# Performance work log

Hardware: AMD Instinct MI355X
Metric: run time of the kernel (lower is better)

Reference implementation:

```python
import jax, jax.numpy as jnp
import numpy as np

NHEAD = 16  # n_head; head_size N = C // NHEAD = 64


def _forward(x, time_maa_x, time_maa, time_maa_w1, time_maa_w2,
             time_decay, time_decay_w1, time_decay_w2,
             time_aaaaa, time_aaa_w1, time_aaa_w2,
             time_kkk_w1, time_kkk_w2,
             gate_w1, gate_w2,
             time_misc_a, ma_w1, ma_w2,
             time_misc_k, mk_w1, mk_w2,
             receptance, key_w, value, output,
             ln_w, ln_b, time_faaaa):
    B, T, C = x.shape
    H, N = NHEAD, C // NHEAD
    # --- fused_time_shift: token shift + 4-way LoRA mixing (rg, wa, k, v) ---
    xprev = jnp.pad(x, ((0, 0), (1, 0), (0, 0)))[:, :T]   # shift right by one token
    xx = xprev - x
    xxx = x + xx * time_maa_x
    mix = jnp.tanh(xxx @ time_maa_w1.T).reshape(B, T, 4, -1)        # (B,T,4,32)
    deltas = jnp.einsum('btfd,fcd->fbtc', mix, time_maa_w2)         # (4,B,T,C)
    xrg, xwa, xk, xv = x[None] + xx[None] * (time_maa + deltas)
    # --- projections + small LoRAs ---
    r = xrg @ receptance.T
    g = jnp.tanh(xrg @ gate_w1.T) @ gate_w2.T                       # gate
    k = xk @ key_w.T
    kk1 = jnp.tanh(xk @ time_kkk_w1.T)
    mk1 = xk @ mk_w1.T
    v = xv @ value.T
    w1 = jnp.tanh(xwa @ time_decay_w1.T)
    a1 = xwa @ time_aaa_w1.T
    ma1 = xwa @ ma_w1.T
    # data-dependent log-decay, clamped <= -0.5 via softplus
    w = -jax.nn.softplus(-(time_decay + w1 @ time_decay_w2.T)) - 0.5
    # removal key kk: per-head L2-normalized
    kk = k + kk1 @ time_kkk_w2.T
    kk = kk.reshape(B, T, H, N)
    kk = kk / jnp.maximum(jnp.linalg.norm(kk, axis=-1, keepdims=True), 1e-12)
    kk = kk.reshape(B, T, C)
    a = jax.nn.sigmoid(time_aaaaa + a1 @ time_aaa_w2.T)
    ma = jax.nn.sigmoid(time_misc_a + ma1 @ ma_w2.T)
    k = k * ma + k * a * (1 - ma)
    mk = jax.nn.sigmoid(time_misc_k + mk1 @ mk_w2.T)
    k = k * jnp.exp(w * mk)
    b = -kk * a
    # --- RWKV-7 linear-attention scan; state S: (B,H,N_value,N_key) ---
    def heads(z):
        return z.reshape(B, T, H, N).transpose(1, 0, 2, 3)          # (T,B,H,N)
    rh, wh, kh, vh, kkh, bh = map(heads, (r, w, k, v, kk, b))

    def step(S, inp):
        r_, w_, k_, v_, kk_, b_ = inp
        sab = jnp.einsum('bhvk,bhk->bhv', S, kk_)                   # S @ kk
        S = (S * jnp.exp(w_)[:, :, None, :]                         # diag decay on key dim
             + sab[..., None] * b_[:, :, None, :]                   # (S kk) b^T  (delta-rule removal)
             + v_[..., None] * k_[:, :, None, :])                   # v k^T
        y = jnp.einsum('bhvk,bhk->bhv', S, r_)
        return S, y

    S0 = jnp.zeros((B, H, N, N), x.dtype)
    _, y = jax.lax.scan(step, S0, (rh, wh, kh, vh, kkh, bh))
    y = y.transpose(1, 0, 2, 3)                                     # (B,T,H,N)
    # --- GroupNorm (H groups, eps=64e-5) + r.k bonus + gate (fused_attn_ln tail) ---
    mu = y.mean(-1, keepdims=True)
    var = ((y - mu) ** 2).mean(-1, keepdims=True)
    yn = (y - mu) / jnp.sqrt(var + 0.00064) * ln_w.reshape(H, N) + ln_b.reshape(H, N)
    r4 = r.reshape(B, T, H, N)
    k4 = k.reshape(B, T, H, N)
    v4 = v.reshape(B, T, H, N)
    bonus = (r4 * k4 * time_faaaa.reshape(H, N)).sum(-1, keepdims=True) * v4
    out = (yn + bonus).reshape(B, T, C) * g
    return out @ output.T


def setup_inputs() -> dict:
    key = jax.random.key(0)
    ks = iter(jax.random.split(key, 40))
    B, T, C = 2, 1024, 1024
    def n(shape, s=1.0):
        return jax.random.normal(next(ks), shape, jnp.float32) * s
    def u(shape, lo, hi):
        return jax.random.uniform(next(ks), shape, jnp.float32, lo, hi)
    d = {}
    d['x'] = n((B, T, C))
    d['time_maa_x'] = u((1, 1, C), 0.0, 1.0)
    d['time_maa'] = u((4, 1, 1, C), 0.0, 1.0)
    d['time_maa_w1'] = n((128, C), 0.02)
    d['time_maa_w2'] = n((4, C, 32), 0.05)
    d['time_decay'] = u((1, 1, C), -6.5, -1.5)
    d['time_decay_w1'] = n((64, C), 0.02)
    d['time_decay_w2'] = n((C, 64), 0.05)
    d['time_aaaaa'] = n((1, 1, C), 0.1)
    d['time_aaa_w1'] = n((16, C), 0.02)
    d['time_aaa_w2'] = n((C, 16), 0.05)
    d['time_kkk_w1'] = n((16, C), 0.02)
    d['time_kkk_w2'] = n((C, 16), 0.05)
    d['gate_w1'] = n((128, C), 0.05)
    d['gate_w2'] = n((C, 128), 0.05)
    d['time_misc_a'] = n((1, 1, C), 0.1)
    d['ma_w1'] = n((16, C), 0.02)
    d['ma_w2'] = n((C, 16), 0.05)
    d['time_misc_k'] = n((1, 1, C), 0.1)
    d['mk_w1'] = n((16, C), 0.02)
    d['mk_w2'] = n((C, 16), 0.05)
    s = 0.5 / C ** 0.5
    d['receptance'] = u((C, C), -s, s)
    d['key_w'] = u((C, C), -0.1 * s, 0.1 * s)
    d['value'] = u((C, C), -s, s)
    d['output'] = n((C, C), 0.02)
    d['ln_w'] = jnp.ones((C,), jnp.float32)
    d['ln_b'] = jnp.zeros((C,), jnp.float32)
    d['time_faaaa'] = n((C,), 0.1)
    return d


def reference(x, time_maa_x, time_maa, time_maa_w1, time_maa_w2,
              time_decay, time_decay_w1, time_decay_w2,
              time_aaaaa, time_aaa_w1, time_aaa_w2,
              time_kkk_w1, time_kkk_w2,
              gate_w1, gate_w2,
              time_misc_a, ma_w1, ma_w2,
              time_misc_k, mk_w1, mk_w2,
              receptance, key_w, value, output,
              ln_w, ln_b, time_faaaa):
    return _forward(x, time_maa_x, time_maa, time_maa_w1, time_maa_w2,
                    time_decay, time_decay_w1, time_decay_w2,
                    time_aaaaa, time_aaa_w1, time_aaa_w2,
                    time_kkk_w1, time_kkk_w2,
                    gate_w1, gate_w2,
                    time_misc_a, ma_w1, ma_w2,
                    time_misc_k, mk_w1, mk_w2,
                    receptance, key_w, value, output,
                    ln_w, ln_b, time_faaaa)
```

## Files before the change

kernel.cpp:

```cpp
#include <hip/hip_runtime.h>
#include <hip/hip_bf16.h>

typedef __hip_bfloat16 bf16;

#define B_ 2
#define T_ 1024
#define C_ 1024
#define H_ 16
#define N_ 64

using short4v = __attribute__((ext_vector_type(4))) short;
using short8 = __attribute__((ext_vector_type(8))) short;
using f32x4 = __attribute__((ext_vector_type(4))) float;

__device__ __forceinline__ float us2f(unsigned short u) {
  return __uint_as_float(((unsigned int)u) << 16);
}
__device__ __forceinline__ float bs2f(short s) {
  return __uint_as_float(((unsigned int)(unsigned short)s) << 16);
}
__device__ __forceinline__ bf16 f2bf(float f) { return __float2bfloat16(f); }
__device__ __forceinline__ short bfbits(float f) {
  bf16 h = __float2bfloat16(f);
  return *reinterpret_cast<short*>(&h);
}
__device__ __forceinline__ float sigmoidf_(float x) { return 1.0f / (1.0f + expf(-x)); }
__device__ __forceinline__ float softplusf_(float x) {
  return fmaxf(x, 0.0f) + log1pf(expf(-fabsf(x)));
}
__device__ __forceinline__ float qsum16(float x) {
  int a = __builtin_amdgcn_update_dpp(0, __float_as_int(x), 0xB1, 0xF, 0xF, true);
  x += __int_as_float(a);
  int b = __builtin_amdgcn_update_dpp(0, __float_as_int(x), 0x4E, 0xF, 0xF, true);
  x += __int_as_float(b);
  int c = __builtin_amdgcn_update_dpp(0, __float_as_int(x), 0x124, 0xF, 0xF, true);
  x += __int_as_float(c);
  int d = __builtin_amdgcn_update_dpp(0, __float_as_int(x), 0x128, 0xF, 0xF, true);
  x += __int_as_float(d);
  return x;
}
__device__ __forceinline__ void qsum16x2(float& x, float& y) {
  int a0 = __builtin_amdgcn_update_dpp(0, __float_as_int(x), 0xB1, 0xF, 0xF, true);
  int b0 = __builtin_amdgcn_update_dpp(0, __float_as_int(y), 0xB1, 0xF, 0xF, true);
  x += __int_as_float(a0); y += __int_as_float(b0);
  int a1 = __builtin_amdgcn_update_dpp(0, __float_as_int(x), 0x4E, 0xF, 0xF, true);
  int b1 = __builtin_amdgcn_update_dpp(0, __float_as_int(y), 0x4E, 0xF, 0xF, true);
  x += __int_as_float(a1); y += __int_as_float(b1);
  int a2 = __builtin_amdgcn_update_dpp(0, __float_as_int(x), 0x124, 0xF, 0xF, true);
  int b2 = __builtin_amdgcn_update_dpp(0, __float_as_int(y), 0x124, 0xF, 0xF, true);
  x += __int_as_float(a2); y += __int_as_float(b2);
  int a3 = __builtin_amdgcn_update_dpp(0, __float_as_int(x), 0x128, 0xF, 0xF, true);
  int b3 = __builtin_amdgcn_update_dpp(0, __float_as_int(y), 0x128, 0xF, 0xF, true);
  x += __int_as_float(a3); y += __int_as_float(b3);
}

__global__ __launch_bounds__(256) void cvt_all_kernel(
    const float* __restrict__ s0, const float* __restrict__ s1,
    const float* __restrict__ s2, const float* __restrict__ s3,
    const float* __restrict__ s4, const float* __restrict__ s5,
    const float* __restrict__ s6,
    bf16* __restrict__ d0, bf16* __restrict__ d1, bf16* __restrict__ d2,
    bf16* __restrict__ d3, bf16* __restrict__ d4, bf16* __restrict__ d5,
    bf16* __restrict__ d6,
    const float* __restrict__ tkw1, const float* __restrict__ mkw1,
    const float* __restrict__ tdw1, const float* __restrict__ taw1,
    const float* __restrict__ maw1,
    bf16* __restrict__ wsk, bf16* __restrict__ wswa,
    const float* __restrict__ tmw2, const float* __restrict__ tdw2,
    const float* __restrict__ tkw2, const float* __restrict__ taw2,
    const float* __restrict__ maw2, const float* __restrict__ mkw2,
    bf16* __restrict__ tmw2e, bf16* __restrict__ tdw2b,
    bf16* __restrict__ tkw2b, bf16* __restrict__ taw2b,
    bf16* __restrict__ maw2b, bf16* __restrict__ mkw2b) {
  long bidx = blockIdx.x;
  const float* s; bf16* d; long off;
  if (bidx < 4480) {
    long i4 = bidx * 256 + threadIdx.x;
    if (i4 < 32768) { s = s0; d = d0; off = i4; }
    else if (i4 < 294912) { s = s1; d = d1; off = i4 - 32768; }
    else if (i4 < 327680) { s = s2; d = d2; off = i4 - 294912; }
    else if (i4 < 360448) { s = s3; d = d3; off = i4 - 327680; }
    else if (i4 < 622592) { s = s4; d = d4; off = i4 - 360448; }
    else if (i4 < 884736) { s = s5; d = d5; off = i4 - 622592; }
    else { s = s6; d = d6; off = i4 - 884736; }
  } else if (bidx < 4608) {
    long i4 = (bidx - 4480) * 256 + threadIdx.x;
    long so, dof;
    if (i4 < 4096) { s = tkw1; so = i4; d = wsk; dof = i4; }
    else if (i4 < 8192) { s = mkw1; so = i4 - 4096; d = wsk; dof = i4; }
    else if (i4 < 24576) { s = tdw1; so = i4 - 8192; d = wswa; dof = i4 - 8192; }
    else if (i4 < 28672) { s = taw1; so = i4 - 24576; d = wswa; dof = i4 - 8192; }
    else { s = maw1; so = i4 - 28672; d = wswa; dof = i4 - 8192; }
    float4 v = *(const float4*)(s + so * 4);
    d[dof * 4 + 0] = f2bf(v.x); d[dof * 4 + 1] = f2bf(v.y);
    d[dof * 4 + 2] = f2bf(v.z); d[dof * 4 + 3] = f2bf(v.w);
    return;
  } else if (bidx < 4736) {
    long i4 = (bidx - 4608) * 256 + threadIdx.x;
    if (i4 < 16384) { s = tdw2; d = tdw2b; off = i4; }
    else if (i4 < 20480) { s = tkw2; d = tkw2b; off = i4 - 16384; }
    else if (i4 < 24576) { s = taw2; d = taw2b; off = i4 - 20480; }
    else if (i4 < 28672) { s = maw2; d = maw2b; off = i4 - 24576; }
    else { s = mkw2; d = mkw2b; off = i4 - 28672; }
  } else {
    long i4 = (bidx - 4736) * 256 + threadIdx.x;
    long n = i4 >> 5;
    int k0 = (int)(i4 & 31) << 2;
    int f = (int)(n >> 10);
    float4 v = {0.f, 0.f, 0.f, 0.f};
    if ((k0 >> 5) == f) v = *(const float4*)(tmw2 + n * 32 + (k0 & 31));
    tmw2e[i4 * 4 + 0] = f2bf(v.x);
    tmw2e[i4 * 4 + 1] = f2bf(v.y);
    tmw2e[i4 * 4 + 2] = f2bf(v.z);
    tmw2e[i4 * 4 + 3] = f2bf(v.w);
    return;
  }
  float4 v = *(const float4*)(s + off * 4);
  d[off * 4 + 0] = f2bf(v.x);
  d[off * 4 + 1] = f2bf(v.y);
  d[off * 4 + 2] = f2bf(v.z);
  d[off * 4 + 3] = f2bf(v.w);
}

struct GemmBatch {
  const bf16* A[6]; const bf16* W[6];
  float* Cf[6]; bf16* Cb[6];
  int N[6]; int actN[6];
};

__global__ __launch_bounds__(256) void gemm_batch_kernel(GemmBatch gb, int K) {
  __shared__ __align__(16) bf16 As[128][72];
  __shared__ __align__(16) bf16 Ws[64][72];
  int z = blockIdx.z;
  int Nz = gb.N[z];
  int n0 = blockIdx.x << 6;
  if (n0 >= Nz) return;
  int m0 = blockIdx.y << 7;
  int actN = gb.actN[z];
  const bf16* A = gb.A[z];
  const bf16* W = gb.W[z];
  float* Cf = gb.Cf[z];
  bf16* Cb = gb.Cb[z];
  int tid = threadIdx.x;
  int arow = tid >> 1, acol = (tid & 1) << 5;
  int wrow = tid >> 2, wcol = (tid & 3) << 4;
  int wv = tid >> 6, lane = tid & 63;
  int fr = lane & 15, fq = lane >> 4;
  bool wok = (n0 + wrow) < Nz;
  const bf16* Ap = A + (long)(m0 + arow) * K + acol;
  const bf16* Wp = W + (long)(n0 + wrow) * K + wcol;
  short8 zz = {0, 0, 0, 0, 0, 0, 0, 0};
  f32x4 a00 = {0.f, 0.f, 0.f, 0.f};
  f32x4 a01 = a00, a02 = a00, a03 = a00, a10 = a00, a11 = a00, a12 = a00, a13 = a00;
  for (int k0 = 0; k0 < K; k0 += 64) {
    *(short8*)&As[arow][acol] = *(const short8*)(Ap + k0);
    *(short8*)&As[arow][acol + 8] = *(const short8*)(Ap + k0 + 8);
    *(short8*)&As[arow][acol + 16] = *(const short8*)(Ap + k0 + 16);
    *(short8*)&As[arow][acol + 24] = *(const short8*)(Ap + k0 + 24);
    *(short8*)&Ws[wrow][wcol] = wok ? *(const short8*)(Wp + k0) : zz;
    *(short8*)&Ws[wrow][wcol + 8] = wok ? *(const short8*)(Wp + k0 + 8) : zz;
    __syncthreads();
#pragma unroll
    for (int kk = 0; kk < 2; kk++) {
      int ko = (fq << 3) + (kk << 5);
      short8 af0 = *(const short8*)&As[(wv << 5) + fr][ko];
      short8 af1 = *(const short8*)&As[(wv << 5) + 16 + fr][ko];
      short8 b0 = *(const short8*)&Ws[fr][ko];
      short8 b1 = *(const short8*)&Ws[16 + fr][ko];
      short8 b2 = *(const short8*)&Ws[32 + fr][ko];
      short8 b3 = *(const short8*)&Ws[48 + fr][ko];
      a00 = __builtin_amdgcn_mfma_f32_16x16x32_bf16(af0, b0, a00, 0, 0, 0);
      a01 = __builtin_amdgcn_mfma_f32_16x16x32_bf16(af0, b1, a01, 0, 0, 0);
      a02 = __builtin_amdgcn_mfma_f32_16x16x32_bf16(af0, b2, a02, 0, 0, 0);
      a03 = __builtin_amdgcn_mfma_f32_16x16x32_bf16(af0, b3, a03, 0, 0, 0);
      a10 = __builtin_amdgcn_mfma_f32_16x16x32_bf16(af1, b0, a10, 0, 0, 0);
      a11 = __builtin_amdgcn_mfma_f32_16x16x32_bf16(af1, b1, a11, 0, 0, 0);
      a12 = __builtin_amdgcn_mfma_f32_16x16x32_bf16(af1, b2, a12, 0, 0, 0);
      a13 = __builtin_amdgcn_mfma_f32_16x16x32_bf16(af1, b3, a13, 0, 0, 0);
    }
    __syncthreads();
  }
  int ocol = n0 + fr;
  int orow0 = m0 + (wv << 5) + (fq << 2);
#define WRB(accv, mf, nt) { int col = ocol + ((nt) << 4); if (col < Nz) { \
    _Pragma("unroll") for (int r = 0; r < 4; r++) { \
      float vvv = accv[r]; if (col < actN) vvv = tanhf(vvv); \
      long oi = (long)(orow0 + ((mf) << 4) + r) * Nz + col; \
      if (Cb) Cb[oi] = f2bf(vvv); else Cf[oi] = vvv; } } }
  WRB(a00, 0, 0) WRB(a01, 0, 1) WRB(a02, 0, 2) WRB(a03, 0, 3)
  WRB(a10, 1, 0) WRB(a11, 1, 1) WRB(a12, 1, 2) WRB(a13, 1, 3)
#undef WRB
}

__global__ __launch_bounds__(256) void gemm_mix_kernel(
    const float* __restrict__ x, const float* __restrict__ tmx,
    const bf16* __restrict__ W, bf16* __restrict__ Cb) {
  __shared__ __align__(16) bf16 As[128][72];
  __shared__ __align__(16) bf16 Ws[64][72];
  const int K = 1024;
  int n0 = blockIdx.x << 6;
  int m0 = blockIdx.y << 7;
  int tid = threadIdx.x;
  int arow = tid >> 1, acol = (tid & 1) << 5;
  int wrow = tid >> 2, wcol = (tid & 3) << 4;
  int wv = tid >> 6, lane = tid & 63;
  int fr = lane & 15, fq = lane >> 4;
  int grow = m0 + arow;
  int t = grow & (T_ - 1);
  const float* xp = x + (long)grow * C_ + acol;
  const bf16* Wp = W + (long)(n0 + wrow) * K + wcol;
  f32x4 a00 = {0.f, 0.f, 0.f, 0.f};
  f32x4 a01 = a00, a02 = a00, a03 = a00, a10 = a00, a11 = a00, a12 = a00, a13 = a00;
  for (int k0 = 0; k0 < K; k0 += 64) {
#pragma unroll
    for (int jj = 0; jj < 4; jj++) {
      int co = k0 + (jj << 3);
      float4 c0 = *(const float4*)(xp + co);
      float4 c1 = *(const float4*)(xp + co + 4);
      float4 q0 = {0.f, 0.f, 0.f, 0.f}, q1 = q0;
      if (t > 0) {
        q0 = *(const float4*)(xp + co - C_);
        q1 = *(const float4*)(xp + co + 4 - C_);
      }
      float4 m0v = *(const float4*)(tmx + co + acol);
      float4 m1v = *(const float4*)(tmx + co + acol + 4);
      short8 sv;
      sv[0] = bfbits(fmaf(q0.x - c0.x, m0v.x, c0.x));
      sv[1] = bfbits(fmaf(q0.y - c0.y, m0v.y, c0.y));
      sv[2] = bfbits(fmaf(q0.z - c0.z, m0v.z, c0.z));
      sv[3] = bfbits(fmaf(q0.w - c0.w, m0v.w, c0.w));
      sv[4] = bfbits(fmaf(q1.x - c1.x, m1v.x, c1.x));
      sv[5] = bfbits(fmaf(q1.y - c1.y, m1v.y, c1.y));
      sv[6] = bfbits(fmaf(q1.z - c1.z, m1v.z, c1.z));
      sv[7] = bfbits(fmaf(q1.w - c1.w, m1v.w, c1.w));
      *(short8*)&As[arow][acol + (jj << 3)] = sv;
    }
    *(short8*)&Ws[wrow][wcol] = *(const short8*)(Wp + k0);
    *(short8*)&Ws[wrow][wcol + 8] = *(const short8*)(Wp + k0 + 8);
    __syncthreads();
#pragma unroll
    for (int kk = 0; kk < 2; kk++) {
      int ko = (fq << 3) + (kk << 5);
      short8 af0 = *(const short8*)&As[(wv << 5) + fr][ko];
      short8 af1 = *(const short8*)&As[(wv << 5) + 16 + fr][ko];
      short8 b0 = *(const short8*)&Ws[fr][ko];
      short8 b1 = *(const short8*)&Ws[16 + fr][ko];
      short8 b2 = *(const short8*)&Ws[32 + fr][ko];
      short8 b3 = *(const short8*)&Ws[48 + fr][ko];
      a00 = __builtin_amdgcn_mfma_f32_16x16x32_bf16(af0, b0, a00, 0, 0, 0);
      a01 = __builtin_amdgcn_mfma_f32_16x16x32_bf16(af0, b1, a01, 0, 0, 0);
      a02 = __builtin_amdgcn_mfma_f32_16x16x32_bf16(af0, b2, a02, 0, 0, 0);
      a03 = __builtin_amdgcn_mfma_f32_16x16x32_bf16(af0, b3, a03, 0, 0, 0);
      a10 = __builtin_amdgcn_mfma_f32_16x16x32_bf16(af1, b0, a10, 0, 0, 0);
      a11 = __builtin_amdgcn_mfma_f32_16x16x32_bf16(af1, b1, a11, 0, 0, 0);
      a12 = __builtin_amdgcn_mfma_f32_16x16x32_bf16(af1, b2, a12, 0, 0, 0);
      a13 = __builtin_amdgcn_mfma_f32_16x16x32_bf16(af1, b3, a13, 0, 0, 0);
    }
    __syncthreads();
  }
  const int Nz = 128;
  int ocol = n0 + fr;
  int orow0 = m0 + (wv << 5) + (fq << 2);
#define WRM(accv, mf, nt) { int col = ocol + ((nt) << 4); \
    _Pragma("unroll") for (int r = 0; r < 4; r++) { \
      long oi = (long)(orow0 + ((mf) << 4) + r) * Nz + col; \
      Cb[oi] = f2bf(tanhf(accv[r])); } }
  WRM(a00, 0, 0) WRM(a01, 0, 1) WRM(a02, 0, 2) WRM(a03, 0, 3)
  WRM(a10, 1, 0) WRM(a11, 1, 1) WRM(a12, 1, 2) WRM(a13, 1, 3)
#undef WRM
}

__global__ __launch_bounds__(256) void apply_mix_kernel(
    const float* __restrict__ x, const bf16* __restrict__ deltas,
    const float* __restrict__ tmaa,
    bf16* __restrict__ xrg, bf16* __restrict__ xwa,
    bf16* __restrict__ xk, bf16* __restrict__ xv) {
  long i4 = (long)blockIdx.x * 256 + threadIdx.x;
  int m = (int)(i4 >> 8);
  int cq = (int)(i4 & 255) << 2;
  int t = m & (T_ - 1);
  long xo = (long)m * C_ + cq;
  float4 xb = *(const float4*)(x + xo);
  float4 xp = {0.f, 0.f, 0.f, 0.f};
  if (t > 0) xp = *(const float4*)(x + xo - C_);
  float4 xxv = {xp.x - xb.x, xp.y - xb.y, xp.z - xb.z, xp.w - xb.w};
  bf16* outs[4] = {xrg, xwa, xk, xv};
#pragma unroll
  for (int f = 0; f < 4; f++) {
    short4v dl = *(const short4v*)(deltas + (long)m * 4096 + (f << 10) + cq);
    float4 ta = *(const float4*)(tmaa + f * C_ + cq);
    short4v sv;
    sv[0] = bfbits(fmaf(xxv.x, ta.x + bs2f(dl[0]), xb.x));
    sv[1] = bfbits(fmaf(xxv.y, ta.y + bs2f(dl[1]), xb.y));
    sv[2] = bfbits(fmaf(xxv.z, ta.z + bs2f(dl[2]), xb.z));
    sv[3] = bfbits(fmaf(xxv.w, ta.w + bs2f(dl[3]), xb.w));
    *(short4v*)(outs[f] + xo) = sv;
  }
}

__global__ __launch_bounds__(256) void fuse2_kernel(
    const float* __restrict__ kraw, const float* __restrict__ out1,
    const float* __restrict__ out2,
    const bf16* __restrict__ dw2, const bf16* __restrict__ kkw2,
    const bf16* __restrict__ aw2, const bf16* __restrict__ maw2,
    const bf16* __restrict__ mkw2,
    const float* __restrict__ tdec, const float* __restrict__ taa,
    const float* __restrict__ tma, const float* __restrict__ tmk,
    float* __restrict__ ew, float* __restrict__ kfin,
    float* __restrict__ kkn, float* __restrict__ bbo) {
  int m = blockIdx.x, tid = threadIdx.x;
  __shared__ float w1r[64], kk1r[16], a1r[16], ma1r[16], mk1r[16];
  if (tid < 64) w1r[tid] = out2[(long)m * 96 + tid];
  else if (tid < 80) kk1r[tid - 64] = out1[(long)m * 32 + (tid - 64)];
  else if (tid < 96) a1r[tid - 80] = out2[(long)m * 96 + 64 + (tid - 80)];
  else if (tid < 112) ma1r[tid - 96] = out2[(long)m * 96 + 80 + (tid - 96)];
  else if (tid < 128) mk1r[tid - 112] = out1[(long)m * 32 + 16 + (tid - 112)];
  __syncthreads();
  float kkp[4], av[4], wv[4], kr[4], mkv[4];
  float sumsq = 0.f;
#pragma unroll
  for (int j = 0; j < 4; j++) {
    int c = (tid << 2) + j;
    long off = (long)m * C_ + c;
    float wd = 0.f;
    const short8* dp = (const short8*)(dw2 + ((long)c << 6));
#pragma unroll
    for (int d8 = 0; d8 < 8; d8++) {
      short8 u = dp[d8];
      int db = d8 << 3;
#pragma unroll
      for (int e = 0; e < 8; e++) wd += w1r[db + e] * bs2f(u[e]);
    }
    float w = -softplusf_(-(tdec[c] + wd)) - 0.5f;
    wv[j] = w;
    float kd = 0.f, ad = 0.f, mad = 0.f, mkd = 0.f;
    const short8* kp = (const short8*)(kkw2 + ((long)c << 4));
    const short8* ap = (const short8*)(aw2 + ((long)c << 4));
    const short8* mp = (const short8*)(maw2 + ((long)c << 4));
    const short8* qp = (const short8*)(mkw2 + ((long)c << 4));
#pragma unroll
    for (int d8 = 0; d8 < 2; d8++) {
      short8 u1 = kp[d8], u2 = ap[d8], u3 = mp[d8], u4 = qp[d8];
      int db = d8 << 3;
#pragma unroll
      for (int e = 0; e < 8; e++) {
        kd += kk1r[db + e] * bs2f(u1[e]);
        ad += a1r[db + e] * bs2f(u2[e]);
        mad += ma1r[db + e] * bs2f(u3[e]);
        mkd += mk1r[db + e] * bs2f(u4[e]);
      }
    }
    float krw = kraw[off];
    float kkpre = krw + kd;
    kkp[j] = kkpre;
    sumsq += kkpre * kkpre;
    float a = sigmoidf_(taa[c] + ad);
    av[j] = a;
    float ma = sigmoidf_(tma[c] + mad);
    float mk = sigmoidf_(tmk[c] + mkd);
    mkv[j] = mk;
    kr[j] = krw * (ma + a * (1.f - ma));
  }
  sumsq += __shfl_xor(sumsq, 1);
  sumsq += __shfl_xor(sumsq, 2);
  sumsq += __shfl_xor(sumsq, 4);
  sumsq += __shfl_xor(sumsq, 8);
  float rn = 1.0f / fmaxf(sqrtf(sumsq), 1e-12f);
#pragma unroll
  for (int j = 0; j < 4; j++) {
    int c = (tid << 2) + j;
    long off = (long)m * C_ + c;
    float kknv = kkp[j] * rn;
    kkn[off] = kknv;
    bbo[off] = -kknv * av[j];
    ew[off] = expf(wv[j]);
    kfin[off] = kr[j] * expf(wv[j] * mkv[j]);
  }
}

#define SCHUNK 16
#define NCHUNK (T_ / SCHUNK)
__global__ __launch_bounds__(256, 1) void scan_kernel(
    const float* __restrict__ rB, const float* __restrict__ ewB,
    const float* __restrict__ kB, const float* __restrict__ vB,
    const float* __restrict__ kkB, const float* __restrict__ bbB,
    float* __restrict__ yB) {
  __shared__ __align__(16) float lds[2][6][SCHUNK * 64];
  int bid = blockIdx.x;
  int bh = bid >> 2, rg = bid & 3;
  int b = bh >> 4, h = bh & 15;
  int tid = threadIdx.x;
  int wave = tid >> 6, lane = tid & 63;
  int g = lane >> 4, q = lane & 15;
  int row = (rg << 4) + (wave << 2) + g;
  int kq = q << 2;
  const long base = ((long)b * T_) * C_ + (h << 6);
  const float* s0 = kkB + base;
  const float* s1 = ewB + base;
  const float* s2 = kB + base;
  const float* s3 = bbB + base;
  const float* s4 = rB + base;
  const float* s5 = vB + base;
  int stok = tid >> 4;
  int spc = (tid & 15) << 2;
  int lo = (stok << 6) + spc;
  float4 rb0, rb1, rb2, rb3, rb4, rb5;
  auto loadc = [&](int c) {
    long go = (long)((c << 4) + stok) * C_ + spc;
    rb0 = *(const float4*)(s0 + go);
    rb1 = *(const float4*)(s1 + go);
    rb2 = *(const float4*)(s2 + go);
    rb3 = *(const float4*)(s3 + go);
    rb4 = *(const float4*)(s4 + go);
    rb5 = *(const float4*)(s5 + go);
  };
  auto stage = [&](int buf) {
    *(float4*)&lds[buf][0][lo] = rb0;
    *(float4*)&lds[buf][1][lo] = rb1;
    *(float4*)&lds[buf][2][lo] = rb2;
    *(float4*)&lds[buf][3][lo] = rb3;
    *(float4*)&lds[buf][4][lo] = rb4;
    *(float4*)&lds[buf][5][lo] = rb5;
  };
  float S0 = 0.f, S1 = 0.f, S2 = 0.f, S3 = 0.f;
  float ypv = 0.f;
  float4 Q0kk, Q0ew, Q0k, Q0bb, Q0r; float Q0v;
  float4 Q1kk, Q1ew, Q1k, Q1bb, Q1r; float Q1v;
  float4 Q2kk, Q2ew, Q2k, Q2bb, Q2r; float Q2v;

#define PF(i, tt) { int tb_ = ((tt) << 6); \
    Q##i##kk = *(const float4*)&lds[cur][0][tb_ + kq]; \
    Q##i##ew = *(const float4*)&lds[cur][1][tb_ + kq]; \
    Q##i##k  = *(const float4*)&lds[cur][2][tb_ + kq]; \
    Q##i##bb = *(const float4*)&lds[cur][3][tb_ + kq]; \
    Q##i##r  = *(const float4*)&lds[cur][4][tb_ + kq]; \
    Q##i##v  = lds[cur][5][tb_ + row]; }
#define SBAR __builtin_amdgcn_sched_barrier(0x7)
#define ST(i, gtok, FIRSTT) { \
    float p_ = fmaf(S1, Q##i##kk.y, S0 * Q##i##kk.x) + \
               fmaf(S3, Q##i##kk.w, S2 * Q##i##kk.z); \
    float yo_ = ypv; \
    qsum16x2(p_, yo_); \
    if (q == 0 && !((FIRSTT) && c == 0)) \
      yB[base + (long)((gtok) - 1) * C_ + row] = yo_; \
    float n0 = fmaf(S0, Q##i##ew.x, Q##i##v * Q##i##k.x); \
    float n1 = fmaf(S1, Q##i##ew.y, Q##i##v * Q##i##k.y); \
    float n2 = fmaf(S2, Q##i##ew.z, Q##i##v * Q##i##k.z); \
    float n3 = fmaf(S3, Q##i##ew.w, Q##i##v * Q##i##k.w); \
    S0 = fmaf(p_, Q##i##bb.x, n0); \
    S1 = fmaf(p_, Q##i##bb.y, n1); \
    S2 = fmaf(p_, Q##i##bb.z, n2); \
    S3 = fmaf(p_, Q##i##bb.w, n3); \
    ypv = fmaf(S1, Q##i##r.y, S0 * Q##i##r.x) + \
          fmaf(S3, Q##i##r.w, S2 * Q##i##r.z); }

  loadc(0);
  stage(0);
  loadc(1);
  __syncthreads();
  int cur = 0;
// ... 14 lines not shown
    PF(1, 10); SBAR; ST(2, t0 + 8, false);
    PF(2, 11); SBAR; ST(0, t0 + 9, false);
    PF(0, 12); SBAR; ST(1, t0 + 10, false);
    PF(1, 13); SBAR; ST(2, t0 + 11, false);
    PF(2, 14); SBAR; ST(0, t0 + 12, false);
    PF(0, 15); SBAR; ST(1, t0 + 13, false);
    ST(2, t0 + 14, false);
    ST(0, t0 + 15, false);
    __syncthreads();
    cur ^= 1;
  }
  {
    float yo = qsum16(ypv);
    if (q == 0) yB[base + (long)(T_ - 1) * C_ + row] = yo;
  }
#undef PF
#undef SBAR
#undef ST
}

__global__ __launch_bounds__(256) void gnout_kernel(
    const float* __restrict__ y, const float* __restrict__ r,
    const float* __restrict__ kf, const float* __restrict__ v,
    const float* __restrict__ g,
    const float* __restrict__ lnw, const float* __restrict__ lnb,
    const float* __restrict__ fa, bf16* __restrict__ z) {
  int tid = threadIdx.x;
  int w = tid >> 6, lane = tid & 63;
  int gi = (blockIdx.x << 2) + w;
  int h = gi & 15, mt = gi >> 4;
  long off = (long)mt * C_ + (h << 6) + lane;
  float yv = y[off];
  float s = yv;
  s += __shfl_xor(s, 1); s += __shfl_xor(s, 2); s += __shfl_xor(s, 4);
  s += __shfl_xor(s, 8); s += __shfl_xor(s, 16); s += __shfl_xor(s, 32);
  float mu = s * (1.0f / 64.0f);
  float d = yv - mu;
  float s2 = d * d;
  s2 += __shfl_xor(s2, 1); s2 += __shfl_xor(s2, 2); s2 += __shfl_xor(s2, 4);
  s2 += __shfl_xor(s2, 8); s2 += __shfl_xor(s2, 16); s2 += __shfl_xor(s2, 32);
  float var = s2 * (1.0f / 64.0f);
  int hc = (h << 6) + lane;
  float dot = r[off] * kf[off] * fa[hc];
  dot += __shfl_xor(dot, 1); dot += __shfl_xor(dot, 2); dot += __shfl_xor(dot, 4);
  dot += __shfl_xor(dot, 8); dot += __shfl_xor(dot, 16); dot += __shfl_xor(dot, 32);
  float yn = d * rsqrtf(var + 0.00064f) * lnw[hc] + lnb[hc];
  z[off] = f2bf((yn + dot * v[off]) * g[off]);
}

extern "C" void kernel_launch(void* const* d_in, const int* in_sizes, int n_in,
                              void* d_out, int out_size, void* d_ws, size_t ws_size,
                              hipStream_t stream) {
  const float* x = (const float*)d_in[0];
  const float* tmx = (const float*)d_in[1];
  const float* tmaa = (const float*)d_in[2];
  const float* tmw1 = (const float*)d_in[3];
  const float* tmw2 = (const float*)d_in[4];
  const float* tdec = (const float*)d_in[5];
  const float* tdw1 = (const float*)d_in[6];
  const float* tdw2 = (const float*)d_in[7];
  const float* taa5 = (const float*)d_in[8];
  const float* taw1 = (const float*)d_in[9];
  const float* taw2 = (const float*)d_in[10];
  const float* tkw1 = (const float*)d_in[11];
  const float* tkw2 = (const float*)d_in[12];
  const float* gw1 = (const float*)d_in[13];
  const float* gw2 = (const float*)d_in[14];
  const float* tmia = (const float*)d_in[15];
  const float* maw1 = (const float*)d_in[16];
  const float* maw2 = (const float*)d_in[17];
  const float* tmik = (const float*)d_in[18];
  const float* mkw1 = (const float*)d_in[19];
  const float* mkw2 = (const float*)d_in[20];
  const float* wrec = (const float*)d_in[21];
  const float* wkey = (const float*)d_in[22];
  const float* wval = (const float*)d_in[23];
  const float* wout = (const float*)d_in[24];
  const float* lnw = (const float*)d_in[25];
  const float* lnb = (const float*)d_in[26];
  const float* faaa = (const float*)d_in[27];

  const long MT = 2048, CC = 1024;
  char* base = (char*)d_ws;
  float* xx = (float*)base;    base += MT * CC * 4;
  bf16* xxxb = (bf16*)base;    base += MT * CC * 2;
  bf16* xrgb = (bf16*)base;    base += MT * CC * 2;
  bf16* xwab = (bf16*)base;    base += MT * CC * 2;
  bf16* xkb = (bf16*)base;     base += MT * CC * 2;
  bf16* xvb = (bf16*)base;     base += MT * CC * 2;
  float* rr = (float*)base;    base += MT * CC * 4;
  float* kraw = (float*)base;  base += MT * CC * 4;
  float* vv = (float*)base;    base += MT * CC * 4;
  float* gg = (float*)base;    base += MT * CC * 4;
  float* bbo = (float*)base;   base += MT * CC * 4;
  float* mix = (float*)base;   base += MT * 128 * 4;
  bf16* g1b = (bf16*)base;     base += MT * 128 * 2;
  float* out1 = (float*)base;  base += MT * 32 * 4;
  float* out2 = (float*)base;  base += MT * 96 * 4;
  bf16* zb = (bf16*)base;      base += MT * CC * 2;
  bf16* tmw1b = (bf16*)base;   base += 128 * CC * 2;
  bf16* wrecb = (bf16*)base;   base += CC * CC * 2;
  bf16* gw1b = (bf16*)base;    base += 128 * CC * 2;
  bf16* gw2b = (bf16*)base;    base += CC * 128 * 2;
  bf16* wkeyb = (bf16*)base;   base += CC * CC * 2;
  bf16* wvalb = (bf16*)base;   base += CC * CC * 2;
  bf16* woutb = (bf16*)base;   base += CC * CC * 2;
  bf16* wskb = (bf16*)base;    base += 32 * CC * 2;
  bf16* wswab = (bf16*)base;   base += 96 * CC * 2;
  bf16* tmw2b = (bf16*)base;   base += 4 * CC * 32 * 2;
  bf16* tdw2b = (bf16*)base;   base += CC * 64 * 2;
  bf16* tkw2b = (bf16*)base;   base += CC * 16 * 2;
  bf16* taw2b = (bf16*)base;   base += CC * 16 * 2;
  bf16* maw2b = (bf16*)base;   base += CC * 16 * 2;
  bf16* mkw2b = (bf16*)base;   base += CC * 16 * 2;
  bf16* mixb = (bf16*)base;    base += MT * 128 * 2;
  bf16* tmw2e = (bf16*)base;   base += 4096L * 128 * 2;
  bf16* deltasb = (bf16*)base; base += MT * 4096L * 2;
  float* ew = kraw;
  float* kfin = (float*)xrgb;
  float* kkn = (float*)xkb;
  float* y = xx;
  (void)xxxb; (void)mix; (void)tmw2b;

  cvt_all_kernel<<<5248, 256, 0, stream>>>(
      tmw1, wrec, gw1, gw2, wkey, wval, wout,
      tmw1b, wrecb, gw1b, gw2b, wkeyb, wvalb, woutb,
      tkw1, mkw1, tdw1, taw1, maw1, wskb, wswab,
      tmw2, tdw2, tkw2, taw2, maw2, mkw2,
      tmw2e, tdw2b, tkw2b, taw2b, maw2b, mkw2b);

  gemm_mix_kernel<<<dim3(2, 16), 256, 0, stream>>>(x, tmx, tmw1b, mixb);
  {
    GemmBatch gb = {};
    gb.A[0] = mixb; gb.W[0] = tmw2e; gb.Cf[0] = nullptr; gb.Cb[0] = deltasb;
    gb.N[0] = 4096; gb.actN[0] = 0;
    gemm_batch_kernel<<<dim3(64, 16, 1), 256, 0, stream>>>(gb, 128);
  }
  apply_mix_kernel<<<2048, 256, 0, stream>>>(x, deltasb, tmaa,
                                             xrgb, xwab, xkb, xvb);
  {
    GemmBatch gb = {};
    gb.A[0] = xrgb; gb.W[0] = wrecb; gb.Cf[0] = rr;   gb.Cb[0] = nullptr; gb.N[0] = 1024; gb.actN[0] = 0;
    gb.A[1] = xrgb; gb.W[1] = gw1b;  gb.Cf[1] = nullptr; gb.Cb[1] = g1b;  gb.N[1] = 128;  gb.actN[1] = 128;
    gb.A[2] = xkb;  gb.W[2] = wkeyb; gb.Cf[2] = kraw; gb.Cb[2] = nullptr; gb.N[2] = 1024; gb.actN[2] = 0;
    gb.A[3] = xkb;  gb.W[3] = wskb;  gb.Cf[3] = out1; gb.Cb[3] = nullptr; gb.N[3] = 32;   gb.actN[3] = 16;
    gb.A[4] = xvb;  gb.W[4] = wvalb; gb.Cf[4] = vv;   gb.Cb[4] = nullptr; gb.N[4] = 1024; gb.actN[4] = 0;
    gb.A[5] = xwab; gb.W[5] = wswab; gb.Cf[5] = out2; gb.Cb[5] = nullptr; gb.N[5] = 96;   gb.actN[5] = 64;
    gemm_batch_kernel<<<dim3(16, 16, 6), 256, 0, stream>>>(gb, 1024);
  }
  {
    GemmBatch gb = {};
    gb.A[0] = g1b; gb.W[0] = gw2b; gb.Cf[0] = gg; gb.Cb[0] = nullptr;
    gb.N[0] = 1024; gb.actN[0] = 0;
    gemm_batch_kernel<<<dim3(16, 16, 1), 256, 0, stream>>>(gb, 128);
  }
  fuse2_kernel<<<2048, 256, 0, stream>>>(kraw, out1, out2,
                                         tdw2b, tkw2b, taw2b, maw2b, mkw2b,
                                         tdec, taa5, tmia, tmik,
                                         ew, kfin, kkn, bbo);
  scan_kernel<<<128, 256, 0, stream>>>(rr, ew, kfin, vv, kkn, bbo, y);
  gnout_kernel<<<8192, 256, 0, stream>>>(y, rr, kfin, vv, gg, lnw, lnb, faaa, zb);
  {
    GemmBatch gb = {};
    gb.A[0] = zb; gb.W[0] = woutb; gb.Cf[0] = (float*)d_out; gb.Cb[0] = nullptr;
    gb.N[0] = 1024; gb.actN[0] = 0;
    gemm_batch_kernel<<<dim3(16, 16, 1), 256, 0, stream>>>(gb, 1024);
  }
}
```

Measured before the change: 522.7 us.

## Fuse mix-delta GEMM with apply step and move small LoRA up-projections to MFMA GEMM

The deltas GEMM epilogue now applies the token-shift mixing directly, so the bf16 deltas buffer no longer goes through global memory and the separate apply kernel is gone. The five small second-stage LoRA projections (decay, a, ma, kkk, mk) are packed into a block-structured 5120x128 weight and computed by the batched MFMA GEMM, replacing scalar dot products inside fuse2. fuse2 then becomes a vectorised elementwise kernel that reads a large fp32 d2 buffer. The trade-off is extra zero-padded MFMA work and the traffic to write and read d2, plus an epilogue in the fused kernel that does scattered scalar x loads.

Result: faster. 429.5 us (-17.8%).

```diff
diff --git a/kernel.cpp b/kernel.cpp
--- a/kernel.cpp
+++ b/kernel.cpp
@@ -13,9 +13,6 @@
 using short8 = __attribute__((ext_vector_type(8))) short;
 using f32x4 = __attribute__((ext_vector_type(4))) float;
 
-__device__ __forceinline__ float us2f(unsigned short u) {
-  return __uint_as_float(((unsigned int)u) << 16);
-}
 __device__ __forceinline__ float bs2f(short s) {
   return __uint_as_float(((unsigned int)(unsigned short)s) << 16);
 }
@@ -59,7 +56,7 @@
     const float* __restrict__ s2, const float* __restrict__ s3,
     const float* __restrict__ s4, const float* __restrict__ s5,
     const float* __restrict__ s6,
-    bf16* __restrict__ d0, bf16* __restrict__ d1, bf16* __restrict__ d2,
+    bf16* __restrict__ d0, bf16* __restrict__ d1, bf16* __restrict__ d2w,
     bf16* __restrict__ d3, bf16* __restrict__ d4, bf16* __restrict__ d5,
     bf16* __restrict__ d6,
     const float* __restrict__ tkw1, const float* __restrict__ mkw1,
@@ -69,16 +66,14 @@
     const float* __restrict__ tmw2, const float* __restrict__ tdw2,
     const float* __restrict__ tkw2, const float* __restrict__ taw2,
     const float* __restrict__ maw2, const float* __restrict__ mkw2,
-    bf16* __restrict__ tmw2e, bf16* __restrict__ tdw2b,
-    bf16* __restrict__ tkw2b, bf16* __restrict__ taw2b,
-    bf16* __restrict__ maw2b, bf16* __restrict__ mkw2b) {
+    bf16* __restrict__ tmw2e, bf16* __restrict__ w2e5) {
   long bidx = blockIdx.x;
   const float* s; bf16* d; long off;
   if (bidx < 4480) {
     long i4 = bidx * 256 + threadIdx.x;
     if (i4 < 32768) { s = s0; d = d0; off = i4; }
     else if (i4 < 294912) { s = s1; d = d1; off = i4 - 32768; }
-    else if (i4 < 327680) { s = s2; d = d2; off = i4 - 294912; }
+    else if (i4 < 327680) { s = s2; d = d2w; off = i4 - 294912; }
     else if (i4 < 360448) { s = s3; d = d3; off = i4 - 327680; }
     else if (i4 < 622592) { s = s4; d = d4; off = i4 - 360448; }
     else if (i4 < 884736) { s = s5; d = d5; off = i4 - 622592; }
@@ -95,15 +90,8 @@
     d[dof * 4 + 0] = f2bf(v.x); d[dof * 4 + 1] = f2bf(v.y);
     d[dof * 4 + 2] = f2bf(v.z); d[dof * 4 + 3] = f2bf(v.w);
     return;
-  } else if (bidx < 4736) {
+  } else if (bidx < 5120) {
     long i4 = (bidx - 4608) * 256 + threadIdx.x;
-    if (i4 < 16384) { s = tdw2; d = tdw2b; off = i4; }
-    else if (i4 < 20480) { s = tkw2; d = tkw2b; off = i4 - 16384; }
-    else if (i4 < 24576) { s = taw2; d = taw2b; off = i4 - 20480; }
-    else if (i4 < 28672) { s = maw2; d = maw2b; off = i4 - 24576; }
-    else { s = mkw2; d = mkw2b; off = i4 - 28672; }
-  } else {
-    long i4 = (bidx - 4736) * 256 + threadIdx.x;
     long n = i4 >> 5;
     int k0 = (int)(i4 & 31) << 2;
     int f = (int)(n >> 10);
@@ -114,6 +102,23 @@
     tmw2e[i4 * 4 + 2] = f2bf(v.z);
     tmw2e[i4 * 4 + 3] = f2bf(v.w);
     return;
+  } else {
+    long i4 = (bidx - 5120) * 256 + threadIdx.x;
+    long rowi = i4 >> 5;
+    int k0 = (int)(i4 & 31) << 2;
+    int j = (int)(rowi >> 10);
+    int c = (int)(rowi & 1023);
+    float4 v = {0.f, 0.f, 0.f, 0.f};
+    if (j == 0) { if (k0 < 64) v = *(const float4*)(tdw2 + c * 64 + k0); }
+    else if (j == 1) { if (k0 >= 64 && k0 < 80) v = *(const float4*)(taw2 + c * 16 + (k0 - 64)); }
+    else if (j == 2) { if (k0 >= 80 && k0 < 96) v = *(const float4*)(maw2 + c * 16 + (k0 - 80)); }
+    else if (j == 3) { if (k0 >= 96 && k0 < 112) v = *(const float4*)(tkw2 + c * 16 + (k0 - 96)); }
+    else { if (k0 >= 112) v = *(const float4*)(mkw2 + c * 16 + (k0 - 112)); }
+    w2e5[i4 * 4 + 0] = f2bf(v.x);
+    w2e5[i4 * 4 + 1] = f2bf(v.y);
+    w2e5[i4 * 4 + 2] = f2bf(v.z);
+    w2e5[i4 * 4 + 3] = f2bf(v.w);
+    return;
   }
   float4 v = *(const float4*)(s + off * 4);
   d[off * 4 + 0] = f2bf(v.x);
@@ -125,7 +130,7 @@
 struct GemmBatch {
   const bf16* A[6]; const bf16* W[6];
   float* Cf[6]; bf16* Cb[6];
-  int N[6]; int actN[6];
+  int N[6]; int actN[6]; int ldc[6]; int coff[6];
 };
 
 __global__ __launch_bounds__(256) void gemm_batch_kernel(GemmBatch gb, int K) {
@@ -137,6 +142,7 @@
   if (n0 >= Nz) return;
   int m0 = blockIdx.y << 7;
   int actN = gb.actN[z];
+  int ldc = gb.ldc[z], coff = gb.coff[z];
   const bf16* A = gb.A[z];
   const bf16* W = gb.W[z];
   float* Cf = gb.Cf[z];
@@ -185,7 +191,7 @@
 #define WRB(accv, mf, nt) { int col = ocol + ((nt) << 4); if (col < Nz) { \
     _Pragma("unroll") for (int r = 0; r < 4; r++) { \
       float vvv = accv[r]; if (col < actN) vvv = tanhf(vvv); \
-      long oi = (long)(orow0 + ((mf) << 4) + r) * Nz + col; \
+      long oi = (long)(orow0 + ((mf) << 4) + r) * ldc + coff + col; \
       if (Cb) Cb[oi] = f2bf(vvv); else Cf[oi] = vvv; } } }
   WRB(a00, 0, 0) WRB(a01, 0, 1) WRB(a02, 0, 2) WRB(a03, 0, 3)
   WRB(a10, 1, 0) WRB(a11, 1, 1) WRB(a12, 1, 2) WRB(a13, 1, 3)
@@ -270,112 +276,140 @@
 #undef WRM
 }
 
-__global__ __launch_bounds__(256) void apply_mix_kernel(
-    const float* __restrict__ x, const bf16* __restrict__ deltas,
-    const float* __restrict__ tmaa,
+__global__ __launch_bounds__(256) void gemm_mixapply_kernel(
+    const bf16* __restrict__ A, const bf16* __restrict__ W,
+    const float* __restrict__ x, const float* __restrict__ tmaa,
     bf16* __restrict__ xrg, bf16* __restrict__ xwa,
     bf16* __restrict__ xk, bf16* __restrict__ xv) {
-  long i4 = (long)blockIdx.x * 256 + threadIdx.x;
-  int m = (int)(i4 >> 8);
-  int cq = (int)(i4 & 255) << 2;
-  int t = m & (T_ - 1);
-  long xo = (long)m * C_ + cq;
-  float4 xb = *(const float4*)(x + xo);
-  float4 xp = {0.f, 0.f, 0.f, 0.f};
-  if (t > 0) xp = *(const float4*)(x + xo - C_);
-  float4 xxv = {xp.x - xb.x, xp.y - xb.y, xp.z - xb.z, xp.w - xb.w};
-  bf16* outs[4] = {xrg, xwa, xk, xv};
+  __shared__ __align__(16) bf16 As[128][72];
+  __shared__ __align__(16) bf16 Ws[64][72];
+  const int K = 128;
+  int n0 = blockIdx.x << 6;
+  int m0 = blockIdx.y << 7;
+  int tid = threadIdx.x;
+  int arow = tid >> 1, acol = (tid & 1) << 5;
+  int wrow = tid >> 2, wcol = (tid & 3) << 4;
+  int wv = tid >> 6, lane = tid & 63;
+  int fr = lane & 15, fq = lane >> 4;
+  const bf16* Ap = A + (long)(m0 + arow) * K + acol;
+  const bf16* Wp = W + (long)(n0 + wrow) * K + wcol;
+  f32x4 a00 = {0.f, 0.f, 0.f, 0.f};
+  f32x4 a01 = a00, a02 = a00, a03 = a00, a10 = a00, a11 = a00, a12 = a00, a13 = a00;
+  for (int k0 = 0; k0 < K; k0 += 64) {
+    *(short8*)&As[arow][acol] = *(const short8*)(Ap + k0);
+    *(short8*)&As[arow][acol + 8] = *(const short8*)(Ap + k0 + 8);
+    *(short8*)&As[arow][acol + 16] = *(const short8*)(Ap + k0 + 16);
+    *(short8*)&As[arow][acol + 24] = *(const short8*)(Ap + k0 + 24);
+    *(short8*)&Ws[wrow][wcol] = *(const short8*)(Wp + k0);
+    *(short8*)&Ws[wrow][wcol + 8] = *(const short8*)(Wp + k0 + 8);
+    __syncthreads();
 #pragma unroll
-  for (int f = 0; f < 4; f++) {
-    short4v dl = *(const short4v*)(deltas + (long)m * 4096 + (f << 10) + cq);
-    float4 ta = *(const float4*)(tmaa + f * C_ + cq);
-    short4v sv;
-    sv[0] = bfbits(fmaf(xxv.x, ta.x + bs2f(dl[0]), xb.x));
-    sv[1] = bfbits(fmaf(xxv.y, ta.y + bs2f(dl[1]), xb.y));
-    sv[2] = bfbits(fmaf(xxv.z, ta.z + bs2f(dl[2]), xb.z));
-    sv[3] = bfbits(fmaf(xxv.w, ta.w + bs2f(dl[3]), xb.w));
-    *(short4v*)(outs[f] + xo) = sv;
-  }
+    for (int kk = 0; kk < 2; kk++) {
+      int ko = (fq << 3) + (kk << 5);
+      short8 af0 = *(const short8*)&As[(wv << 5) + fr][ko];
+      short8 af1 = *(const short8*)&As[(wv << 5) + 16 + fr][ko];
+      short8 b0 = *(const short8*)&Ws[fr][ko];
+      short8 b1 = *(const short8*)&Ws[16 + fr][ko];
+      short8 b2 = *(const short8*)&Ws[32 + fr][ko];
+      short8 b3 = *(const short8*)&Ws[48 + fr][ko];
+      a00 = __builtin_amdgcn_mfma_f32_16x16x32_bf16(af0, b0, a00, 0, 0, 0);
+      a01 = __builtin_amdgcn_mfma_f32_16x16x32_bf16(af0, b1, a01, 0, 0, 0);
+      a02 = __builtin_amdgcn_mfma_f32_16x16x32_bf16(af0, b2, a02, 0, 0, 0);
+      a03 = __builtin_amdgcn_mfma_f32_16x16x32_bf16(af0, b3, a03, 0, 0, 0);
+      a10 = __builtin_amdgcn_mfma_f32_16x16x32_bf16(af1, b0, a10, 0, 0, 0);
+      a11 = __builtin_amdgcn_mfma_f32_16x16x32_bf16(af1, b1, a11, 0, 0, 0);
+      a12 = __builtin_amdgcn_mfma_f32_16x16x32_bf16(af1, b2, a12, 0, 0, 0);
+      a13 = __builtin_amdgcn_mfma_f32_16x16x32_bf16(af1, b3, a13, 0, 0, 0);
+    }
+    __syncthreads();
+  }
+  int f = n0 >> 10;
+  int c0 = n0 & 1023;
+  bf16* outp = (f == 0) ? xrg : (f == 1) ? xwa : (f == 2) ? xk : xv;
+  int ocol = c0 + fr;
+  int orow0 = m0 + (wv << 5) + (fq << 2);
+#define WRA(accv, mf, nt) { int cc = ocol + ((nt) << 4); \
+    float ta = tmaa[(f << 10) + cc]; \
+    _Pragma("unroll") for (int r = 0; r < 4; r++) { \
+      int row = orow0 + ((mf) << 4) + r; \
+      int t = row & (T_ - 1); \
+      long xo = (long)row * C_ + cc; \
+      float xb = x[xo]; \
+      float xq = (t > 0) ? x[xo - C_] : 0.0f; \
+      outp[xo] = f2bf(fmaf(xq - xb, ta + accv[r], xb)); } }
+  WRA(a00, 0, 0) WRA(a01, 0, 1) WRA(a02, 0, 2) WRA(a03, 0, 3)
+  WRA(a10, 1, 0) WRA(a11, 1, 1) WRA(a12, 1, 2) WRA(a13, 1, 3)
+#undef WRA
 }
 
 __global__ __launch_bounds__(256) void fuse2_kernel(
-    const float* __restrict__ kraw, const float* __restrict__ out1,
-    const float* __restrict__ out2,
-    const bf16* __restrict__ dw2, const bf16* __restrict__ kkw2,
-    const bf16* __restrict__ aw2, const bf16* __restrict__ maw2,
-    const bf16* __restrict__ mkw2,
+    const float* __restrict__ kraw, const float* __restrict__ d2,
     const float* __restrict__ tdec, const float* __restrict__ taa,
     const float* __restrict__ tma, const float* __restrict__ tmk,
     float* __restrict__ ew, float* __restrict__ kfin,
     float* __restrict__ kkn, float* __restrict__ bbo) {
   int m = blockIdx.x, tid = threadIdx.x;
-  __shared__ float w1r[64], kk1r[16], a1r[16], ma1r[16], mk1r[16];
-  if (tid < 64) w1r[tid] = out2[(long)m * 96 + tid];
-  else if (tid < 80) kk1r[tid - 64] = out1[(long)m * 32 + (tid - 64)];
-  else if (tid < 96) a1r[tid - 80] = out2[(long)m * 96 + 64 + (tid - 80)];
-  else if (tid < 112) ma1r[tid - 96] = out2[(long)m * 96 + 80 + (tid - 96)];
-  else if (tid < 128) mk1r[tid - 112] = out1[(long)m * 32 + 16 + (tid - 112)];
-  __syncthreads();
-  float kkp[4], av[4], wv[4], kr[4], mkv[4];
+  int c4 = tid << 2;
+  const float* dp = d2 + (long)m * 5120;
+  float4 wd4 = *(const float4*)(dp + c4);
+  float4 ad4 = *(const float4*)(dp + 1024 + c4);
+  float4 mad4 = *(const float4*)(dp + 2048 + c4);
+  float4 kd4 = *(const float4*)(dp + 3072 + c4);
+  float4 mkd4 = *(const float4*)(dp + 4096 + c4);
+  float4 kraw4 = *(const float4*)(kraw + (long)m * C_ + c4);
+  float4 tdec4 = *(const float4*)(tdec + c4);
+  float4 taa4 = *(const float4*)(taa + c4);
+  float4 tma4 = *(const float4*)(tma + c4);
+  float4 tmk4 = *(const float4*)(tmk + c4);
+  float wd[4] = {wd4.x, wd4.y, wd4.z, wd4.w};
+  float ad[4] = {ad4.x, ad4.y, ad4.z, ad4.w};
+  float mad[4] = {mad4.x, mad4.y, mad4.z, mad4.w};
+  float kd[4] = {kd4.x, kd4.y, kd4.z, kd4.w};
+  float mkd[4] = {mkd4.x, mkd4.y, mkd4.z, mkd4.w};
+  float krw[4] = {kraw4.x, kraw4.y, kraw4.z, kraw4.w};
+  float td[4] = {tdec4.x, tdec4.y, tdec4.z, tdec4.w};
+  float ta[4] = {taa4.x, taa4.y, taa4.z, taa4.w};
+  float tm[4] = {tma4.x, tma4.y, tma4.z, tma4.w};
+  float tk[4] = {tmk4.x, tmk4.y, tmk4.z, tmk4.w};
+  float kkp[4], av[4], wvv[4], kr[4], mkv[4];
   float sumsq = 0.f;
 #pragma unroll
   for (int j = 0; j < 4; j++) {
-    int c = (tid << 2) + j;
-    long off = (long)m * C_ + c;
-    float wd = 0.f;
-    const short8* dp = (const short8*)(dw2 + ((long)c << 6));
-#pragma unroll
-    for (int d8 = 0; d8 < 8; d8++) {
-      short8 u = dp[d8];
-      int db = d8 << 3;
-#pragma unroll
-      for (int e = 0; e < 8; e++) wd += w1r[db + e] * bs2f(u[e]);
-    }
-    float w = -softplusf_(-(tdec[c] + wd)) - 0.5f;
-    wv[j] = w;
-    float kd = 0.f, ad = 0.f, mad = 0.f, mkd = 0.f;
-    const short8* kp = (const short8*)(kkw2 + ((long)c << 4));
-    const short8* ap = (const short8*)(aw2 + ((long)c << 4));
-    const short8* mp = (const short8*)(maw2 + ((long)c << 4));
-    const short8* qp = (const short8*)(mkw2 + ((long)c << 4));
-#pragma unroll
-    for (int d8 = 0; d8 < 2; d8++) {
-      short8 u1 = kp[d8], u2 = ap[d8], u3 = mp[d8], u4 = qp[d8];
-      int db = d8 << 3;
-#pragma unroll
-      for (int e = 0; e < 8; e++) {
-        kd += kk1r[db + e] * bs2f(u1[e]);
-        ad += a1r[db + e] * bs2f(u2[e]);
-        mad += ma1r[db + e] * bs2f(u3[e]);
-        mkd += mk1r[db + e] * bs2f(u4[e]);
-      }
-    }
-    float krw = kraw[off];
-    float kkpre = krw + kd;
+    float w = -softplusf_(-(td[j] + wd[j])) - 0.5f;
+    wvv[j] = w;
+    float kkpre = krw[j] + kd[j];
     kkp[j] = kkpre;
     sumsq += kkpre * kkpre;
-    float a = sigmoidf_(taa[c] + ad);
+    float a = sigmoidf_(ta[j] + ad[j]);
     av[j] = a;
-    float ma = sigmoidf_(tma[c] + mad);
-    float mk = sigmoidf_(tmk[c] + mkd);
+    float ma = sigmoidf_(tm[j] + mad[j]);
+    float mk = sigmoidf_(tk[j] + mkd[j]);
     mkv[j] = mk;
-    kr[j] = krw * (ma + a * (1.f - ma));
+    kr[j] = krw[j] * (ma + a * (1.f - ma));
   }
   sumsq += __shfl_xor(sumsq, 1);
   sumsq += __shfl_xor(sumsq, 2);
   sumsq += __shfl_xor(sumsq, 4);
   sumsq += __shfl_xor(sumsq, 8);
   float rn = 1.0f / fmaxf(sqrtf(sumsq), 1e-12f);
+  float4 kknv, bbov, eww, kfv;
+  float* kknp = (float*)&kknv;
+  float* bbop = (float*)&bbov;
+  float* ewp = (float*)&eww;
+  float* kfp = (float*)&kfv;
 #pragma unroll
   for (int j = 0; j < 4; j++) {
-    int c = (tid << 2) + j;
-    long off = (long)m * C_ + c;
-    float kknv = kkp[j] * rn;
-    kkn[off] = kknv;
-    bbo[off] = -kknv * av[j];
-    ew[off] = expf(wv[j]);
-    kfin[off] = kr[j] * expf(wv[j] * mkv[j]);
-  }
+    float kkx = kkp[j] * rn;
+    kknp[j] = kkx;
+    bbop[j] = -kkx * av[j];
+    ewp[j] = expf(wvv[j]);
+    kfp[j] = kr[j] * expf(wvv[j] * mkv[j]);
+  }
+  long off4 = (long)m * C_ + c4;
+  *(float4*)(kkn + off4) = kknv;
+  *(float4*)(bbo + off4) = bbov;
+  *(float4*)(ew + off4) = eww;
+  *(float4*)(kfin + off4) = kfv;
 }
 
 #define SCHUNK 16
@@ -556,8 +590,7 @@
 
   const long MT = 2048, CC = 1024;
   char* base = (char*)d_ws;
-  float* xx = (float*)base;    base += MT * CC * 4;
-  bf16* xxxb = (bf16*)base;    base += MT * CC * 2;
+  float* y = (float*)base;     base += MT * CC * 4;
   bf16* xrgb = (bf16*)base;    base += MT * CC * 2;
   bf16* xwab = (bf16*)base;    base += MT * CC * 2;
   bf16* xkb = (bf16*)base;     base += MT * CC * 2;
@@ -567,11 +600,11 @@
   float* vv = (float*)base;    base += MT * CC * 4;
   float* gg = (float*)base;    base += MT * CC * 4;
   float* bbo = (float*)base;   base += MT * CC * 4;
-  float* mix = (float*)base;   base += MT * 128 * 4;
   bf16* g1b = (bf16*)base;     base += MT * 128 * 2;
-  float* out1 = (float*)base;  base += MT * 32 * 4;
-  float* out2 = (float*)base;  base += MT * 96 * 4;
+  bf16* out12b = (bf16*)base;  base += MT * 128 * 2;
   bf16* zb = (bf16*)base;      base += MT * CC * 2;
+  bf16* mixb = (bf16*)base;    base += MT * 128 * 2;
+  float* d2 = (float*)base;    base += MT * 5120L * 4;
   bf16* tmw1b = (bf16*)base;   base += 128 * CC * 2;
   bf16* wrecb = (bf16*)base;   base += CC * CC * 2;
   bf16* gw1b = (bf16*)base;    base += 128 * CC * 2;
@@ -581,63 +614,46 @@
   bf16* woutb = (bf16*)base;   base += CC * CC * 2;
   bf16* wskb = (bf16*)base;    base += 32 * CC * 2;
   bf16* wswab = (bf16*)base;   base += 96 * CC * 2;
-  bf16* tmw2b = (bf16*)base;   base += 4 * CC * 32 * 2;
-  bf16* tdw2b = (bf16*)base;   base += CC * 64 * 2;
-  bf16* tkw2b = (bf16*)base;   base += CC * 16 * 2;
-  bf16* taw2b = (bf16*)base;   base += CC * 16 * 2;
-  bf16* maw2b = (bf16*)base;   base += CC * 16 * 2;
-  bf16* mkw2b = (bf16*)base;   base += CC * 16 * 2;
-  bf16* mixb = (bf16*)base;    base += MT * 128 * 2;
   bf16* tmw2e = (bf16*)base;   base += 4096L * 128 * 2;
-  bf16* deltasb = (bf16*)base; base += MT * 4096L * 2;
+  bf16* w2e5b = (bf16*)base;   base += 5120L * 128 * 2;
   float* ew = kraw;
   float* kfin = (float*)xrgb;
   float* kkn = (float*)xkb;
-  float* y = xx;
-  (void)xxxb; (void)mix; (void)tmw2b;
-
-  cvt_all_kernel<<<5248, 256, 0, stream>>>(
+
+  cvt_all_kernel<<<5760, 256, 0, stream>>>(
       tmw1, wrec, gw1, gw2, wkey, wval, wout,
       tmw1b, wrecb, gw1b, gw2b, wkeyb, wvalb, woutb,
       tkw1, mkw1, tdw1, taw1, maw1, wskb, wswab,
       tmw2, tdw2, tkw2, taw2, maw2, mkw2,
-      tmw2e, tdw2b, tkw2b, taw2b, maw2b, mkw2b);
+      tmw2e, w2e5b);
 
   gemm_mix_kernel<<<dim3(2, 16), 256, 0, stream>>>(x, tmx, tmw1b, mixb);
+  gemm_mixapply_kernel<<<dim3(64, 16), 256, 0, stream>>>(
+      mixb, tmw2e, x, tmaa, xrgb, xwab, xkb, xvb);
   {
     GemmBatch gb = {};
-    gb.A[0] = mixb; gb.W[0] = tmw2e; gb.Cf[0] = nullptr; gb.Cb[0] = deltasb;
-    gb.N[0] = 4096; gb.actN[0] = 0;
-    gemm_batch_kernel<<<dim3(64, 16, 1), 256, 0, stream>>>(gb, 128);
-  }
-  apply_mix_kernel<<<2048, 256, 0, stream>>>(x, deltasb, tmaa,
-                                             xrgb, xwab, xkb, xvb);
+    gb.A[0] = xrgb; gb.W[0] = wrecb; gb.Cf[0] = rr;      gb.Cb[0] = nullptr; gb.N[0] = 1024; gb.actN[0] = 0;   gb.ldc[0] = 1024; gb.coff[0] = 0;
+    gb.A[1] = xrgb; gb.W[1] = gw1b;  gb.Cf[1] = nullptr; gb.Cb[1] = g1b;     gb.N[1] = 128;  gb.actN[1] = 128; gb.ldc[1] = 128;  gb.coff[1] = 0;
+    gb.A[2] = xkb;  gb.W[2] = wkeyb; gb.Cf[2] = kraw;    gb.Cb[2] = nullptr; gb.N[2] = 1024; gb.actN[2] = 0;   gb.ldc[2] = 1024; gb.coff[2] = 0;
+    gb.A[3] = xkb;  gb.W[3] = wskb;  gb.Cf[3] = nullptr; gb.Cb[3] = out12b;  gb.N[3] = 32;   gb.actN[3] = 16;  gb.ldc[3] = 128;  gb.coff[3] = 96;
+    gb.A[4] = xvb;  gb.W[4] = wvalb; gb.Cf[4] = vv;      gb.Cb[4] = nullptr; gb.N[4] = 1024; gb.actN[4] = 0;   gb.ldc[4] = 1024; gb.coff[4] = 0;
+    gb.A[5] = xwab; gb.W[5] = wswab; gb.Cf[5] = nullptr; gb.Cb[5] = out12b;  gb.N[5] = 96;   gb.actN[5] = 64;  gb.ldc[5] = 128;  gb.coff[5] = 0;
+    gemm_batch_kernel<<<dim3(16, 16, 6), 256, 0, stream>>>(gb, 1024);
+  }
   {
     GemmBatch gb = {};
-    gb.A[0] = xrgb; gb.W[0] = wrecb; gb.Cf[0] = rr;   gb.Cb[0] = nullptr; gb.N[0] = 1024; gb.actN[0] = 0;
-    gb.A[1] = xrgb; gb.W[1] = gw1b;  gb.Cf[1] = nullptr; gb.Cb[1] = g1b;  gb.N[1] = 128;  gb.actN[1] = 128;
-    gb.A[2] = xkb;  gb.W[2] = wkeyb; gb.Cf[2] = kraw; gb.Cb[2] = nullptr; gb.N[2] = 1024; gb.actN[2] = 0;
-    gb.A[3] = xkb;  gb.W[3] = wskb;  gb.Cf[3] = out1; gb.Cb[3] = nullptr; gb.N[3] = 32;   gb.actN[3] = 16;
-    gb.A[4] = xvb;  gb.W[4] = wvalb; gb.Cf[4] = vv;   gb.Cb[4] = nullptr; gb.N[4] = 1024; gb.actN[4] = 0;
-    gb.A[5] = xwab; gb.W[5] = wswab; gb.Cf[5] = out2; gb.Cb[5] = nullptr; gb.N[5] = 96;   gb.actN[5] = 64;
-    gemm_batch_kernel<<<dim3(16, 16, 6), 256, 0, stream>>>(gb, 1024);
-  }
-  {
-    GemmBatch gb = {};
-    gb.A[0] = g1b; gb.W[0] = gw2b; gb.Cf[0] = gg; gb.Cb[0] = nullptr;
-    gb.N[0] = 1024; gb.actN[0] = 0;
-    gemm_batch_kernel<<<dim3(16, 16, 1), 256, 0, stream>>>(gb, 128);
-  }
-  fuse2_kernel<<<2048, 256, 0, stream>>>(kraw, out1, out2,
-                                         tdw2b, tkw2b, taw2b, maw2b, mkw2b,
-                                         tdec, taa5, tmia, tmik,
+    gb.A[0] = g1b;    gb.W[0] = gw2b;  gb.Cf[0] = gg; gb.Cb[0] = nullptr; gb.N[0] = 1024; gb.actN[0] = 0; gb.ldc[0] = 1024; gb.coff[0] = 0;
+    gb.A[1] = out12b; gb.W[1] = w2e5b; gb.Cf[1] = d2; gb.Cb[1] = nullptr; gb.N[1] = 5120; gb.actN[1] = 0; gb.ldc[1] = 5120; gb.coff[1] = 0;
+    gemm_batch_kernel<<<dim3(80, 16, 2), 256, 0, stream>>>(gb, 128);
+  }
+  fuse2_kernel<<<2048, 256, 0, stream>>>(kraw, d2, tdec, taa5, tmia, tmik,
                                          ew, kfin, kkn, bbo);
   scan_kernel<<<128, 256, 0, stream>>>(rr, ew, kfin, vv, kkn, bbo, y);
   gnout_kernel<<<8192, 256, 0, stream>>>(y, rr, kfin, vv, gg, lnw, lnb, faaa, zb);
   {
     GemmBatch gb = {};
     gb.A[0] = zb; gb.W[0] = woutb; gb.Cf[0] = (float*)d_out; gb.Cb[0] = nullptr;
-    gb.N[0] = 1024; gb.actN[0] = 0;
+    gb.N[0] = 1024; gb.actN[0] = 0; gb.ldc[0] = 1024; gb.coff[0] = 0;
     gemm_batch_kernel<<<dim3(16, 16, 1), 256, 0, stream>>>(gb, 1024);
   }
 }
```
